# Kernel tuning notes

Hardware: AMD Instinct MI355X
Metric: run time of the kernel (lower is better)

Reference implementation:

```python
import jax, jax.numpy as jnp
import numpy as np

N = 100000   # nodes
H = 96       # hidden_dim
A = 32       # attn_dim
De = 16      # edge_embeddings_dim
E = 500000   # edges per edge type
NEG_SLOPE = 0.01  # torch F.leaky_relu default


def setup_inputs() -> dict:
    key = jax.random.key(0)
    ks = jax.random.split(key, 24)
    nrm = lambda k, shape, s=1.0: jax.random.normal(k, shape, dtype=jnp.float32) * s
    idx = lambda k: jax.random.randint(k, (E,), 0, N, dtype=jnp.int32)
    Din = 2 * H + De
    return {
        'h': nrm(ks[0], (N, H)),
        'src0': idx(ks[1]), 'dst0': idx(ks[2]),
        'src1': idx(ks[3]), 'dst1': idx(ks[4]),
        'src2': idx(ks[5]), 'dst2': idx(ks[6]),
        'Wm0': nrm(ks[7], (Din, H), Din ** -0.5), 'bm0': jnp.zeros((H,), jnp.float32), 'ef0': nrm(ks[8], (De,)),
        'Wm1': nrm(ks[9], (Din, H), Din ** -0.5), 'bm1': jnp.zeros((H,), jnp.float32), 'ef1': nrm(ks[10], (De,)),
        'Wm2': nrm(ks[11], (Din, H), Din ** -0.5), 'bm2': jnp.zeros((H,), jnp.float32), 'ef2': nrm(ks[12], (De,)),
        'Wn0': nrm(ks[13], (H, A), H ** -0.5), 'Wa0': nrm(ks[14], (2 * A, 1), (2 * A) ** -0.5),
        'Wn1': nrm(ks[15], (H, A), H ** -0.5), 'Wa1': nrm(ks[16], (2 * A, 1), (2 * A) ** -0.5),
        'Wu': nrm(ks[17], (4 * H, H), (4 * H) ** -0.5), 'bu': jnp.zeros((H,), jnp.float32),
    }


def _leaky(x):
    return jnp.where(x > 0, x, NEG_SLOPE * x)


def _edge_msg(h, src, dst, Wm, bm, ef):
    # cat(src_h, dst_h, edge_feature) -> Linear  (dropout p=0, eval mode)
    x = jnp.concatenate([h[src], h[dst], jnp.broadcast_to(ef, (src.shape[0], ef.shape[0]))], axis=-1)
    return x @ Wm + bm  # [E, H]


def _mean_agg(m, dst):
    # fn.mean('m','msg'): per-destination mean over incoming edges
    s = jax.ops.segment_sum(m, dst, num_segments=N)
    c = jax.ops.segment_sum(jnp.ones((m.shape[0],), m.dtype), dst, num_segments=N)
    return s / jnp.maximum(c, 1.0)[:, None]


def _attn_agg(scores, m, dst):
    # per-destination softmax over mailbox (variable-size), then weighted sum
    smax = jax.ops.segment_max(scores, dst, num_segments=N)
    ex = jnp.exp(scores - smax[dst])
    den = jax.ops.segment_sum(ex, dst, num_segments=N)
    num = jax.ops.segment_sum(ex[:, None] * m, dst, num_segments=N)
    return num / jnp.maximum(den, 1e-9)[:, None]


def reference(h, src0, dst0, src1, dst1, src2, dst2,
              Wm0, bm0, ef0, Wm1, bm1, ef1, Wm2, bm2, ef2,
              Wn0, Wa0, Wn1, Wa1, Wu, bu):
    # edge type 0: intra_diff (attention), type 1: inter_diff (attention), type 2: intra_lt (mean)
    m0 = _edge_msg(h, src0, dst0, Wm0, bm0, ef0)
    m1 = _edge_msg(h, src1, dst1, Wm1, bm1, ef1)
    m2 = _edge_msg(h, src2, dst2, Wm2, bm2, ef2)

    z0 = h @ Wn0  # [N, A]
    s0 = _leaky(jnp.concatenate([z0[src0], z0[dst0]], axis=-1) @ Wa0)[:, 0]  # [E]
    z1 = h @ Wn1
    s1 = _leaky(jnp.concatenate([z1[src1], z1[dst1]], axis=-1) @ Wa1)[:, 0]

    msg0 = _attn_agg(s0, m0, dst0)   # [N, H]
    msg1 = _attn_agg(s1, m1, dst1)
    msg2 = _mean_agg(m2, dst2)

    # cross_reducer='stack' then concat over edge-type dim -> [N, 3H]
    mcat = jnp.concatenate([msg0, msg1, msg2], axis=-1)
    # cell node update: Linear(cat(h, m)) + ReLU
    return jax.nn.relu(jnp.concatenate([h, mcat], axis=-1) @ Wu + bu)
```

## Files before the change

kernel.cpp:

```cpp
#include <hip/hip_runtime.h>
#include <hip/hip_bf16.h>
#include <cstdint>

#define NN 100000
#define HH 96
#define AD 32
#define DE 16
#define EE 500000
#define NEG 0.01f

#define GSH 10
#define GSZ 1024
#define KB 98
#define CH 4096
#define BPT 123

typedef __bf16 bf16x8 __attribute__((ext_vector_type(8)));
typedef float  f32x4  __attribute__((ext_vector_type(4)));

__device__ __forceinline__ unsigned short f2b(float x) {
    union { float f; unsigned int u; } v; v.f = x;
    unsigned int r = v.u + 0x7fffu + ((v.u >> 16) & 1u);
    return (unsigned short)(r >> 16);
}
__device__ __forceinline__ float b2f(unsigned short h) {
    union { unsigned int u; float f; } v; v.u = ((unsigned int)h) << 16;
    return v.f;
}

__global__ void prep_kernel(const float* Wm0, const float* bm0, const float* ef0,
                            const float* Wm1, const float* bm1, const float* ef1,
                            const float* Wm2, const float* bm2, const float* ef2,
                            const float* Wn0, const float* Wa0,
                            const float* Wn1, const float* Wa1,
                            const float* Wu,
                            float* cvec, float* wvec,
                            unsigned short* BfN, unsigned short* BfU) {
    const float* Wm[3] = {Wm0, Wm1, Wm2};
    const float* bm[3] = {bm0, bm1, bm2};
    const float* ef[3] = {ef0, ef1, ef2};
    const int total = 288 + 384 + 55296 + 36864;
    for (int i = blockIdx.x * blockDim.x + threadIdx.x; i < total;
         i += gridDim.x * blockDim.x) {
        if (i < 288) {
            int t = i / 96, j = i % 96;
            float s = bm[t][j];
            for (int k = 0; k < DE; ++k) s += ef[t][k] * Wm[t][(2 * HH + k) * HH + j];
            cvec[i] = s;
        } else if (i < 288 + 384) {
            int ii = i - 288;
            int kind = ii / 96, k = ii % 96;
            const float* Wn = (kind < 2) ? Wn0 : Wn1;
            const float* Wa = (kind < 2) ? Wa0 : Wa1;
            int off = (kind & 1) ? AD : 0;
            float s = 0.f;
            for (int a = 0; a < AD; ++a) s += Wn[k * AD + a] * Wa[off + a];
            wvec[ii] = s;
        } else if (i < 288 + 384 + 55296) {
            int ii = i - 672;
            int sec = ii / 9216; int rem = ii % 9216;
            int ksc = rem / 512; int lj = rem % 512;
            int ks = ksc / 6, c = ksc % 6;
            int lane = lj / 8, jj = lj % 8;
            int quad = lane / 16, m = lane % 16;
            int k = ks * 32 + quad * 8 + jj;
            int n = c * 16 + m;
            int mt = (sec < 3) ? sec : sec - 3;
            int rowoff = (sec < 3) ? 0 : HH;
            BfN[ii] = f2b(Wm[mt][(rowoff + k) * HH + n]);
        } else {
            int ii = i - (672 + 55296);
            int ksc = ii / 512; int lj = ii % 512;
            int ks = ksc / 6, c = ksc % 6;
            int lane = lj / 8, jj = lj % 8;
            int quad = lane / 16, m = lane % 16;
            int k = ks * 32 + quad * 8 + jj;
            int n = c * 16 + m;
            BfU[ii] = f2b(Wu[k * HH + n]);
        }
    }
}

__global__ void cast_uv_kernel(const float* __restrict__ h, const float* __restrict__ wvec,
                               unsigned short* __restrict__ hb, float* __restrict__ uv) {
    int lane = threadIdx.x & 31;
    int node = (blockIdx.x * blockDim.x + threadIdx.x) >> 5;
    if (node >= NN) return;
    float h0 = h[node * HH + lane];
    float h1 = h[node * HH + 32 + lane];
    float h2 = h[node * HH + 64 + lane];
    hb[node * HH + lane] = f2b(h0);
    hb[node * HH + 32 + lane] = f2b(h1);
    hb[node * HH + 64 + lane] = f2b(h2);
    float acc[4];
#pragma unroll
    for (int q = 0; q < 4; ++q)
        acc[q] = h0 * wvec[q * 96 + lane] + h1 * wvec[q * 96 + 32 + lane] +
                 h2 * wvec[q * 96 + 64 + lane];
#pragma unroll
    for (int d = 16; d >= 1; d >>= 1)
#pragma unroll
        for (int q = 0; q < 4; ++q) acc[q] += __shfl_down(acc[q], d, 32);
    if (lane == 0) {
#pragma unroll
        for (int q = 0; q < 4; ++q) uv[q * NN + node] = acc[q];
    }
}

__global__ void zero_kernel(float4* __restrict__ p, int n4) {
    for (int i = blockIdx.x * blockDim.x + threadIdx.x; i < n4;
         i += gridDim.x * blockDim.x)
        p[i] = make_float4(0.f, 0.f, 0.f, 0.f);
}

__global__ void bucket_hist(const int* __restrict__ d0, const int* __restrict__ d1,
                            const int* __restrict__ d2, int* __restrict__ bCnt) {
    __shared__ int hist[3 * KB];
    int t = threadIdx.x;
    for (int j = t; j < 3 * KB; j += 256) hist[j] = 0;
    __syncthreads();
    const int total = 3 * EE;
    for (int i = blockIdx.x * blockDim.x + t; i < total; i += gridDim.x * blockDim.x) {
        int ty = i / EE, e = i - ty * EE;
        const int* d = (ty == 0) ? d0 : (ty == 1) ? d1 : d2;
        atomicAdd(&hist[ty * KB + (d[e] >> GSH)], 1);
    }
    __syncthreads();
    for (int j = t; j < 3 * KB; j += 256)
        if (hist[j]) atomicAdd(&bCnt[j], hist[j]);
}

__global__ void bucket_scan(const int* __restrict__ bCnt, int* __restrict__ bBase,
                            int* __restrict__ gCursor, int* __restrict__ rs) {
    __shared__ int hist[3 * KB];
    int t = threadIdx.x;
    if (t < 3 * KB) hist[t] = bCnt[t];
    __syncthreads();
    if (t < 3) {
        int run = 0;
        for (int b = 0; b < KB; ++b) {
            bBase[t * (KB + 1) + b] = run;
            gCursor[t * KB + b] = run;
            run += hist[t * KB + b];
        }
        bBase[t * (KB + 1) + KB] = run;
        rs[(size_t)t * (NN + 1) + NN] = run;
    }
}

__global__ __launch_bounds__(256) void bucket_scatter(
    const int* __restrict__ s0, const int* __restrict__ d0,
    const int* __restrict__ s1, const int* __restrict__ d1,
    const int* __restrict__ s2, const int* __restrict__ d2,
    int* __restrict__ gCursor, unsigned int* __restrict__ binned) {
    __shared__ unsigned int recs[CH];
    __shared__ unsigned short rnk[CH];
    __shared__ unsigned char bkt[CH];
    __shared__ int cnt[KB];
    __shared__ int gpos[KB];
    int t = threadIdx.x;
    int type = blockIdx.x / BPT;
    int chunk = (blockIdx.x % BPT) * CH;
    const int* src = (type == 0) ? s0 : (type == 1) ? s1 : s2;
    const int* dst = (type == 0) ? d0 : (type == 1) ? d1 : d2;
    if (t < KB) cnt[t] = 0;
    __syncthreads();
#pragma unroll
    for (int k = 0; k < CH / 256; ++k) {
        int idx = k * 256 + t;
        int e = chunk + idx;
        if (e < EE) {
            int s = src[e], d = dst[e];
            int b = d >> GSH;
            recs[idx] = ((unsigned int)s << GSH) | (unsigned int)(d & (GSZ - 1));
            bkt[idx] = (unsigned char)b;
            rnk[idx] = (unsigned short)atomicAdd(&cnt[b], 1);
        } else {
            bkt[idx] = 0xFF;
        }
    }
    __syncthreads();
    if (t < KB) {
        int c = cnt[t];
        gpos[t] = (c > 0) ? atomicAdd(&gCursor[type * KB + t], c) : 0;
    }
    __syncthreads();
    unsigned int* bout = binned + (size_t)type * EE;
#pragma unroll
    for (int k = 0; k < CH / 256; ++k) {
        int idx = k * 256 + t;
        unsigned char b = bkt[idx];
        if (b != 0xFF) bout[gpos[b] + rnk[idx]] = recs[idx];
    }
}

__global__ __launch_bounds__(256) void bucket_sort(
    const unsigned int* __restrict__ binned, const int* __restrict__ bBase,
    const float* __restrict__ uv,
    int* __restrict__ rs, int* __restrict__ sorted, float* __restrict__ expw) {
    __shared__ int cnt[GSZ];
    __shared__ int tsum[256];
    int t = threadIdx.x;
    int type = blockIdx.x / KB;
    int b = blockIdx.x % KB;
    int nodeBase = b * GSZ;
    int eb = bBase[type * (KB + 1) + b];
    int en = bBase[type * (KB + 1) + b + 1];
    int n = en - eb;
    const unsigned int* bin = binned + (size_t)type * EE + eb;
#pragma unroll
    for (int k = 0; k < GSZ / 256; ++k) cnt[k * 256 + t] = 0;
    __syncthreads();
    for (int i = t; i < n; i += 256) atomicAdd(&cnt[bin[i] & (GSZ - 1)], 1);
    __syncthreads();
    int v[4], s = 0;
#pragma unroll
    for (int k = 0; k < 4; ++k) { v[k] = cnt[t * 4 + k]; s += v[k]; }
    tsum[t] = s;
    __syncthreads();
    for (int off = 1; off < 256; off <<= 1) {
        int add = (t >= off) ? tsum[t - off] : 0;
        __syncthreads();
        tsum[t] += add;
        __syncthreads();
    }
    int run = tsum[t] - s;
    int offk[4];
#pragma unroll
    for (int k = 0; k < 4; ++k) { offk[k] = run; run += v[k]; }
    int* rsrow = rs + (size_t)type * (NN + 1) + nodeBase;
#pragma unroll
    for (int k = 0; k < 4; ++k) {
        int node = t * 4 + k;
        if (nodeBase + node < NN) rsrow[node] = eb + offk[k];
    }
    __syncthreads();
#pragma unroll
    for (int k = 0; k < 4; ++k) cnt[t * 4 + k] = offk[k];
    __syncthreads();
    int* so = sorted + (size_t)type * EE + eb;
    float* ew = expw + (size_t)type * EE + eb;
    const float* u = uv + 2 * type * NN;
    const float* vv = uv + (2 * type + 1) * NN;
    for (int i = t; i < n; i += 256) {
        unsigned int r = bin[i];
        int dl = r & (GSZ - 1);
        int p = atomicAdd(&cnt[dl], 1);
        int srcn = (int)(r >> GSH);
        so[p] = srcn;
        float wgt = 1.f;
        if (type < 2) {
            float sc = u[srcn] + vv[nodeBase + dl];
            sc = sc > 0.f ? sc : NEG * sc;
            wgt = __expf(sc);
        }
        ew[p] = wgt;
    }
}

__global__ void aggregate_kernel(const int* __restrict__ rsAll, const int* __restrict__ sortedAll,
                                 const float* __restrict__ expwAll,
                                 const unsigned short* __restrict__ hb,
                                 unsigned short* __restrict__ hagg,
                                 float* __restrict__ den) {
    const size_t NH = (size_t)NN * HH;
    int lane = threadIdx.x & 31;
    int node = (blockIdx.x * blockDim.x + threadIdx.x) >> 5;
    if (node >= NN) return;
    int t = blockIdx.y;
    const int* rs = rsAll + (size_t)t * (NN + 1);
    const int* sorted = sortedAll + (size_t)t * EE;
    const float* expw = expwAll + (size_t)t * EE;

    int beg = rs[node], end = rs[node + 1];
    float a0 = 0.f, a1 = 0.f, a2 = 0.f, dn = 0.f;
    for (int base = beg; base < end; base += 32) {
        int batch = end - base;
        if (batch > 32) batch = 32;
        int li = lane < batch ? lane : batch - 1;
        int myS = sorted[base + li];
        float myW = expw[base + li];
#pragma unroll 1
        for (int j = 0; j < batch; j += 8) {
            int rem = batch - j;
            int sI[8];
            float wv[8];
#pragma unroll
            for (int k = 0; k < 8; ++k) {
                int jj = (k < rem ? j + k : j);
                sI[k] = __shfl(myS, jj, 32);
                wv[k] = __shfl(myW, jj, 32);
            }
#pragma unroll
            for (int k = 0; k < 8; ++k) if (k >= rem) wv[k] = 0.f;
            float x0[8], x1[8], x2[8];
#pragma unroll
            for (int k = 0; k < 8; ++k) {
                const unsigned short* pr = hb + (size_t)sI[k] * HH;
                x0[k] = b2f(pr[lane]);
                x1[k] = b2f(pr[lane + 32]);
                x2[k] = b2f(pr[lane + 64]);
            }
#pragma unroll
            for (int k = 0; k < 8; ++k) {
                dn += wv[k];
                a0 += wv[k] * x0[k];
                a1 += wv[k] * x1[k];
                a2 += wv[k] * x2[k];
            }
        }
    }
    float r0 = 0.f, r1 = 0.f, r2 = 0.f;
    if (dn > 0.f) {
        float inv = 1.f / dn;
        r0 = a0 * inv; r1 = a1 * inv; r2 = a2 * inv;
    }
    unsigned short* mr = hagg + (size_t)t * NH + (size_t)node * HH;
    mr[lane] = f2b(r0);
    mr[lane + 32] = f2b(r1);
    mr[lane + 64] = f2b(r2);
    if (lane == 0) den[(size_t)t * NN + node] = dn;
}

#define MSP 296
__global__ __launch_bounds__(256) void fused_update_kernel(
    const unsigned short* __restrict__ hagg, const unsigned short* __restrict__ hb,
    const unsigned short* __restrict__ BfN, const unsigned short* __restrict__ BfU,
    const float* __restrict__ den, const float* __restrict__ cvec,
    const float* __restrict__ bu, float* __restrict__ out) {
    __shared__ unsigned short msgt[4][16][MSP];
    const size_t NH = (size_t)NN * HH;
    int wave = threadIdx.x >> 6;
    int lane = threadIdx.x & 63;
    int quad = lane >> 4, m = lane & 15;
    int blk = blockIdx.x * 4 + wave;
    bool active = (blk < NN / 16);
    int r0 = blk * 16;
    bf16x8 hfrag[3];
    if (active) {
        const unsigned short* hrow = hb + (size_t)(r0 + m) * HH + quad * 8;
#pragma unroll
        for (int ks = 0; ks < 3; ++ks) hfrag[ks] = *(const bf16x8*)(hrow + ks * 32);
#pragma unroll
        for (int t = 0; t < 3; ++t) {
            f32x4 acc[6] = {};
            const unsigned short* harow = hagg + (size_t)t * NH + (size_t)(r0 + m) * HH + quad * 8;
#pragma unroll
            for (int ks = 0; ks < 3; ++ks) {
                bf16x8 af = *(const bf16x8*)(harow + ks * 32);
#pragma unroll
                for (int c = 0; c < 6; ++c) {
                    bf16x8 bfv = *(const bf16x8*)(BfN + (((t * 3 + ks) * 6 + c) << 9) + lane * 8);
                    acc[c] = __builtin_amdgcn_mfma_f32_16x16x32_bf16(af, bfv, acc[c], 0, 0, 0);
                }
            }
#pragma unroll
            for (int ks = 0; ks < 3; ++ks) {
#pragma unroll
                for (int c = 0; c < 6; ++c) {
                    bf16x8 bfv = *(const bf16x8*)(BfN + ((((t + 3) * 3 + ks) * 6 + c) << 9) + lane * 8);
                    acc[c] = __builtin_amdgcn_mfma_f32_16x16x32_bf16(hfrag[ks], bfv, acc[c], 0, 0, 0);
                }
            }
            float dnv[4];
#pragma unroll
            for (int r = 0; r < 4; ++r) dnv[r] = den[(size_t)t * NN + r0 + quad * 4 + r];
#pragma unroll
            for (int c = 0; c < 6; ++c) {
                float cv = cvec[t * 96 + c * 16 + m];
#pragma unroll
                for (int r = 0; r < 4; ++r) {
                    float val = (dnv[r] > 0.f) ? (acc[c][r] + cv) : 0.f;
                    msgt[wave][quad * 4 + r][t * 96 + c * 16 + m] = f2b(val);
                }
            }
        }
    }
    __syncthreads();
    if (active) {
        f32x4 acc2[6] = {};
#pragma unroll
        for (int ks = 0; ks < 12; ++ks) {
            bf16x8 af = (ks < 3) ? hfrag[ks]
                                 : *(const bf16x8*)&msgt[wave][m][(ks - 3) * 32 + quad * 8];
#pragma unroll
            for (int c = 0; c < 6; ++c) {
                bf16x8 bfv = *(const bf16x8*)(BfU + ((ks * 6 + c) << 9) + lane * 8);
                acc2[c] = __builtin_amdgcn_mfma_f32_16x16x32_bf16(af, bfv, acc2[c], 0, 0, 0);
            }
        }
#pragma unroll
        for (int c = 0; c < 6; ++c) {
            float b = bu[c * 16 + m];
#pragma unroll
            for (int r = 0; r < 4; ++r) {
                int row = r0 + quad * 4 + r;
                float v2 = acc2[c][r] + b;
                out[(size_t)row * HH + c * 16 + m] = v2 > 0.f ? v2 : 0.f;
            }
        }
    }
}

extern "C" void kernel_launch(void* const* d_in, const int* in_sizes, int n_in,
                              void* d_out, int out_size, void* d_ws, size_t ws_size,
                              hipStream_t stream) {
    (void)in_sizes; (void)n_in; (void)out_size;
    const float* h   = (const float*)d_in[0];
    const int* srcs[3] = {(const int*)d_in[1], (const int*)d_in[3], (const int*)d_in[5]};
    const int* dsts[3] = {(const int*)d_in[2], (const int*)d_in[4], (const int*)d_in[6]};
    const float* Wm0 = (const float*)d_in[7];
    const float* bm0 = (const float*)d_in[8];
    const float* ef0 = (const float*)d_in[9];
    const float* Wm1 = (const float*)d_in[10];
    const float* bm1 = (const float*)d_in[11];
    const float* ef1 = (const float*)d_in[12];
    const float* Wm2 = (const float*)d_in[13];
    const float* bm2 = (const float*)d_in[14];
    const float* ef2 = (const float*)d_in[15];
    const float* Wn0 = (const float*)d_in[16];
    const float* Wa0 = (const float*)d_in[17];
    const float* Wn1 = (const float*)d_in[18];
    const float* Wa1 = (const float*)d_in[19];
    const float* Wu  = (const float*)d_in[20];
    const float* bu  = (const float*)d_in[21];
    float* out = (float*)d_out;

    const size_t NEED = 98991104;
    if (ws_size < NEED) return;
    char* w = (char*)d_ws;
    unsigned short* hb      = (unsigned short*)(w + 0);
    unsigned short* hagg    = (unsigned short*)(w + 19200000);
    float*          den     = (float*)(w + 76800000);
    float*          uv      = (float*)(w + 78000000);
    float*          cvec    = (float*)(w + 79600000);
    float*          wvec    = (float*)(w + 79601280);
    unsigned short* BfN     = (unsigned short*)(w + 79602816);
    unsigned short* BfU     = (unsigned short*)(w + 79713408);
    int*            bBase   = (int*)(w + 79787136);
    int*            gCursor = (int*)(w + 79788416);
    int*            bCnt    = (int*)(w + 79789696);
    int*            rs      = (int*)(w + 79790976);
    int*            sorted  = (int*)(w + 80991104);
    unsigned int*   binned  = (unsigned int*)(w + 86991104);
    float*          expw    = (float*)(w + 92991104);

    prep_kernel<<<128, 256, 0, stream>>>(Wm0, bm0, ef0, Wm1, bm1, ef1, Wm2, bm2, ef2,
                                         Wn0, Wa0, Wn1, Wa1, Wu, cvec, wvec, BfN, BfU);
    cast_uv_kernel<<<12500, 256, 0, stream>>>(h, wvec, hb, uv);

    zero_kernel<<<1, 256, 0, stream>>>((float4*)bCnt, 80);
    bucket_hist<<<512, 256, 0, stream>>>(dsts[0], dsts[1], dsts[2], bCnt);
    bucket_scan<<<1, 384, 0, stream>>>(bCnt, bBase, gCursor, rs);
    bucket_scatter<<<3 * BPT, 256, 0, stream>>>(srcs[0], dsts[0], srcs[1], dsts[1],
                                                srcs[2], dsts[2], gCursor, binned);
    bucket_sort<<<3 * KB, 256, 0, stream>>>(binned, bBase, uv, rs, sorted, expw);

    aggregate_kernel<<<dim3(12500, 3), 256, 0, stream>>>(rs, sorted, expw, hb, hagg, den);
    fused_update_kernel<<<1563, 256, 0, stream>>>(hagg, hb, BfN, BfU, den, cvec, bu, out);
}
```

Measured before the change: 346.7 us.

## Fold message weights into update weights and merge front-end kernels

Precomputes the products Wm_t·Wu_t, so the output kernel does one fused set of MFMAs per edge type and no longer needs the intermediate message tile in shared memory or a second GEMM pass. Merges the bf16 cast, attention-vector computation, weight prep and destination histogram into a single kernel launch. The histogram now writes per-block partials that the scan sums, which removes the zero kernel and the global atomics. In exchange, the prep blocks do heavier dot products serially, and rounding the folded weights to bf16 changes numerics slightly.

New measurement: 397.8 us. 14.7% more time.

```diff
diff --git a/kernel.cpp b/kernel.cpp
--- a/kernel.cpp
+++ b/kernel.cpp
@@ -15,6 +15,10 @@
 #define CH 4096
 #define BPT 123
 
+#define FB_CAST 12500
+#define FB_PREP 128
+#define FB_HIST 64
+
 typedef __bf16 bf16x8 __attribute__((ext_vector_type(8)));
 typedef float  f32x4  __attribute__((ext_vector_type(4)));
 
@@ -28,113 +32,121 @@
     return v.f;
 }
 
-__global__ void prep_kernel(const float* Wm0, const float* bm0, const float* ef0,
-                            const float* Wm1, const float* bm1, const float* ef1,
-                            const float* Wm2, const float* bm2, const float* ef2,
-                            const float* Wn0, const float* Wa0,
-                            const float* Wn1, const float* Wa1,
-                            const float* Wu,
-                            float* cvec, float* wvec,
-                            unsigned short* BfN, unsigned short* BfU) {
-    const float* Wm[3] = {Wm0, Wm1, Wm2};
-    const float* bm[3] = {bm0, bm1, bm2};
-    const float* ef[3] = {ef0, ef1, ef2};
-    const int total = 288 + 384 + 55296 + 36864;
-    for (int i = blockIdx.x * blockDim.x + threadIdx.x; i < total;
-         i += gridDim.x * blockDim.x) {
-        if (i < 288) {
-            int t = i / 96, j = i % 96;
-            float s = bm[t][j];
-            for (int k = 0; k < DE; ++k) s += ef[t][k] * Wm[t][(2 * HH + k) * HH + j];
-            cvec[i] = s;
-        } else if (i < 288 + 384) {
-            int ii = i - 288;
+__global__ __launch_bounds__(256) void fused_front(
+    const float* __restrict__ h,
+    const float* __restrict__ Wm0, const float* __restrict__ bm0, const float* __restrict__ ef0,
+    const float* __restrict__ Wm1, const float* __restrict__ bm1, const float* __restrict__ ef1,
+    const float* __restrict__ Wm2, const float* __restrict__ bm2, const float* __restrict__ ef2,
+    const float* __restrict__ Wn0, const float* __restrict__ Wa0,
+    const float* __restrict__ Wn1, const float* __restrict__ Wa1,
+    const float* __restrict__ Wu,
+    const int* __restrict__ d0, const int* __restrict__ d1, const int* __restrict__ d2,
+    unsigned short* __restrict__ hb, float* __restrict__ uv,
+    unsigned short* __restrict__ BfC, float* __restrict__ cu,
+    int* __restrict__ bCntPart) {
+    int bid = blockIdx.x;
+    int tid = threadIdx.x;
+    if (bid < FB_CAST) {
+        __shared__ float wl[384];
+        for (int ii = tid; ii < 384; ii += 256) {
             int kind = ii / 96, k = ii % 96;
             const float* Wn = (kind < 2) ? Wn0 : Wn1;
             const float* Wa = (kind < 2) ? Wa0 : Wa1;
             int off = (kind & 1) ? AD : 0;
             float s = 0.f;
             for (int a = 0; a < AD; ++a) s += Wn[k * AD + a] * Wa[off + a];
-            wvec[ii] = s;
-        } else if (i < 288 + 384 + 55296) {
-            int ii = i - 672;
-            int sec = ii / 9216; int rem = ii % 9216;
-            int ksc = rem / 512; int lj = rem % 512;
-            int ks = ksc / 6, c = ksc % 6;
-            int lane = lj / 8, jj = lj % 8;
-            int quad = lane / 16, m = lane % 16;
-            int k = ks * 32 + quad * 8 + jj;
-            int n = c * 16 + m;
-            int mt = (sec < 3) ? sec : sec - 3;
-            int rowoff = (sec < 3) ? 0 : HH;
-            BfN[ii] = f2b(Wm[mt][(rowoff + k) * HH + n]);
-        } else {
-            int ii = i - (672 + 55296);
-            int ksc = ii / 512; int lj = ii % 512;
-            int ks = ksc / 6, c = ksc % 6;
-            int lane = lj / 8, jj = lj % 8;
-            int quad = lane / 16, m = lane % 16;
-            int k = ks * 32 + quad * 8 + jj;
-            int n = c * 16 + m;
-            BfU[ii] = f2b(Wu[k * HH + n]);
-        }
-    }
-}
-
-__global__ void cast_uv_kernel(const float* __restrict__ h, const float* __restrict__ wvec,
-                               unsigned short* __restrict__ hb, float* __restrict__ uv) {
-    int lane = threadIdx.x & 31;
-    int node = (blockIdx.x * blockDim.x + threadIdx.x) >> 5;
-    if (node >= NN) return;
-    float h0 = h[node * HH + lane];
-    float h1 = h[node * HH + 32 + lane];
-    float h2 = h[node * HH + 64 + lane];
-    hb[node * HH + lane] = f2b(h0);
-    hb[node * HH + 32 + lane] = f2b(h1);
-    hb[node * HH + 64 + lane] = f2b(h2);
-    float acc[4];
-#pragma unroll
-    for (int q = 0; q < 4; ++q)
-        acc[q] = h0 * wvec[q * 96 + lane] + h1 * wvec[q * 96 + 32 + lane] +
-                 h2 * wvec[q * 96 + 64 + lane];
-#pragma unroll
-    for (int d = 16; d >= 1; d >>= 1)
-#pragma unroll
-        for (int q = 0; q < 4; ++q) acc[q] += __shfl_down(acc[q], d, 32);
-    if (lane == 0) {
-#pragma unroll
-        for (int q = 0; q < 4; ++q) uv[q * NN + node] = acc[q];
-    }
-}
-
-__global__ void zero_kernel(float4* __restrict__ p, int n4) {
-    for (int i = blockIdx.x * blockDim.x + threadIdx.x; i < n4;
-         i += gridDim.x * blockDim.x)
-        p[i] = make_float4(0.f, 0.f, 0.f, 0.f);
-}
-
-__global__ void bucket_hist(const int* __restrict__ d0, const int* __restrict__ d1,
-                            const int* __restrict__ d2, int* __restrict__ bCnt) {
-    __shared__ int hist[3 * KB];
-    int t = threadIdx.x;
-    for (int j = t; j < 3 * KB; j += 256) hist[j] = 0;
-    __syncthreads();
-    const int total = 3 * EE;
-    for (int i = blockIdx.x * blockDim.x + t; i < total; i += gridDim.x * blockDim.x) {
-        int ty = i / EE, e = i - ty * EE;
-        const int* d = (ty == 0) ? d0 : (ty == 1) ? d1 : d2;
-        atomicAdd(&hist[ty * KB + (d[e] >> GSH)], 1);
-    }
-    __syncthreads();
-    for (int j = t; j < 3 * KB; j += 256)
-        if (hist[j]) atomicAdd(&bCnt[j], hist[j]);
-}
-
-__global__ void bucket_scan(const int* __restrict__ bCnt, int* __restrict__ bBase,
+            wl[ii] = s;
+        }
+        __syncthreads();
+        int lane = tid & 31;
+        int node = (bid * 256 + tid) >> 5;
+        float h0 = h[node * HH + lane];
+        float h1 = h[node * HH + 32 + lane];
+        float h2 = h[node * HH + 64 + lane];
+        hb[node * HH + lane] = f2b(h0);
+        hb[node * HH + 32 + lane] = f2b(h1);
+        hb[node * HH + 64 + lane] = f2b(h2);
+        float acc[4];
+#pragma unroll
+        for (int q = 0; q < 4; ++q)
+            acc[q] = h0 * wl[q * 96 + lane] + h1 * wl[q * 96 + 32 + lane] +
+                     h2 * wl[q * 96 + 64 + lane];
+#pragma unroll
+        for (int d = 16; d >= 1; d >>= 1)
+#pragma unroll
+            for (int q = 0; q < 4; ++q) acc[q] += __shfl_down(acc[q], d, 32);
+        if (lane == 0) {
+#pragma unroll
+            for (int q = 0; q < 4; ++q) uv[q * NN + node] = acc[q];
+        }
+    } else if (bid < FB_CAST + FB_PREP) {
+        const float* Wm[3] = {Wm0, Wm1, Wm2};
+        const float* bm[3] = {bm0, bm1, bm2};
+        const float* ef[3] = {ef0, ef1, ef2};
+        const int total = 7 * 9216 + 288;
+        for (int i = (bid - FB_CAST) * 256 + tid; i < total; i += FB_PREP * 256) {
+            if (i < 7 * 9216) {
+                int sec = i / 9216, rem = i % 9216;
+                int ksc = rem / 512, lj = rem % 512;
+                int ks = ksc / 6, c = ksc % 6;
+                int lane = lj / 8, j = lj % 8;
+                int quad = lane / 16, mm = lane % 16;
+                int k = ks * 32 + quad * 8 + j;
+                int n = c * 16 + mm;
+                float val;
+                if (sec == 0) {
+                    val = Wu[k * HH + n];
+                } else if (sec < 4) {
+                    int t = sec - 1;
+                    const float* W = Wm[t];
+                    val = 0.f;
+                    for (int jj = 0; jj < 96; ++jj)
+                        val += W[k * HH + jj] * Wu[(96 + 96 * t + jj) * HH + n];
+                } else {
+                    int t = sec - 4;
+                    const float* W = Wm[t];
+                    val = 0.f;
+                    for (int jj = 0; jj < 96; ++jj)
+                        val += W[(96 + k) * HH + jj] * Wu[(96 + 96 * t + jj) * HH + n];
+                }
+                BfC[i] = f2b(val);
+            } else {
+                int ii = i - 7 * 9216;
+                int t = ii / 96, n = ii % 96;
+                float s = 0.f;
+                for (int k = 0; k < 96; ++k) {
+                    float ct = bm[t][k];
+                    for (int j = 0; j < DE; ++j) ct += ef[t][j] * Wm[t][(192 + j) * HH + k];
+                    s += ct * Wu[(96 + 96 * t + k) * HH + n];
+                }
+                cu[ii] = s;
+            }
+        }
+    } else {
+        __shared__ int hl[3 * KB];
+        int hblk = bid - (FB_CAST + FB_PREP);
+        for (int j = tid; j < 3 * KB; j += 256) hl[j] = 0;
+        __syncthreads();
+        const int total = 3 * EE;
+        for (int i = hblk * 256 + tid; i < total; i += FB_HIST * 256) {
+            int ty = i / EE, e = i - ty * EE;
+            const int* d = (ty == 0) ? d0 : (ty == 1) ? d1 : d2;
+            atomicAdd(&hl[ty * KB + (d[e] >> GSH)], 1);
+        }
+        __syncthreads();
+        for (int j = tid; j < 3 * KB; j += 256) bCntPart[hblk * (3 * KB) + j] = hl[j];
+    }
+}
+
+__global__ void bucket_scan(const int* __restrict__ bCntPart, int* __restrict__ bBase,
                             int* __restrict__ gCursor, int* __restrict__ rs) {
     __shared__ int hist[3 * KB];
     int t = threadIdx.x;
-    if (t < 3 * KB) hist[t] = bCnt[t];
+    if (t < 3 * KB) {
+        int s = 0;
+        for (int b = 0; b < FB_HIST; ++b) s += bCntPart[b * (3 * KB) + t];
+        hist[t] = s;
+    }
     __syncthreads();
     if (t < 3) {
         int run = 0;
@@ -322,82 +334,69 @@
     if (lane == 0) den[(size_t)t * NN + node] = dn;
 }
 
-#define MSP 296
-__global__ __launch_bounds__(256) void fused_update_kernel(
+__global__ __launch_bounds__(256) void fused_out_kernel(
     const unsigned short* __restrict__ hagg, const unsigned short* __restrict__ hb,
-    const unsigned short* __restrict__ BfN, const unsigned short* __restrict__ BfU,
-    const float* __restrict__ den, const float* __restrict__ cvec,
-    const float* __restrict__ bu, float* __restrict__ out) {
-    __shared__ unsigned short msgt[4][16][MSP];
+    const unsigned short* __restrict__ BfC, const float* __restrict__ cu,
+    const float* __restrict__ den, const float* __restrict__ bu,
+    float* __restrict__ out) {
     const size_t NH = (size_t)NN * HH;
     int wave = threadIdx.x >> 6;
     int lane = threadIdx.x & 63;
     int quad = lane >> 4, m = lane & 15;
     int blk = blockIdx.x * 4 + wave;
-    bool active = (blk < NN / 16);
+    if (blk >= NN / 16) return;
     int r0 = blk * 16;
     bf16x8 hfrag[3];
-    if (active) {
-        const unsigned short* hrow = hb + (size_t)(r0 + m) * HH + quad * 8;
-#pragma unroll
-        for (int ks = 0; ks < 3; ++ks) hfrag[ks] = *(const bf16x8*)(hrow + ks * 32);
-#pragma unroll
-        for (int t = 0; t < 3; ++t) {
-            f32x4 acc[6] = {};
-            const unsigned short* harow = hagg + (size_t)t * NH + (size_t)(r0 + m) * HH + quad * 8;
-#pragma unroll
-            for (int ks = 0; ks < 3; ++ks) {
-                bf16x8 af = *(const bf16x8*)(harow + ks * 32);
-#pragma unroll
-                for (int c = 0; c < 6; ++c) {
-                    bf16x8 bfv = *(const bf16x8*)(BfN + (((t * 3 + ks) * 6 + c) << 9) + lane * 8);
-                    acc[c] = __builtin_amdgcn_mfma_f32_16x16x32_bf16(af, bfv, acc[c], 0, 0, 0);
-                }
-            }
-#pragma unroll
-            for (int ks = 0; ks < 3; ++ks) {
-#pragma unroll
-                for (int c = 0; c < 6; ++c) {
-                    bf16x8 bfv = *(const bf16x8*)(BfN + ((((t + 3) * 3 + ks) * 6 + c) << 9) + lane * 8);
-                    acc[c] = __builtin_amdgcn_mfma_f32_16x16x32_bf16(hfrag[ks], bfv, acc[c], 0, 0, 0);
-                }
-            }
-            float dnv[4];
-#pragma unroll
-            for (int r = 0; r < 4; ++r) dnv[r] = den[(size_t)t * NN + r0 + quad * 4 + r];
+    const unsigned short* hrow = hb + (size_t)(r0 + m) * HH + quad * 8;
+#pragma unroll
+    for (int ks = 0; ks < 3; ++ks) hfrag[ks] = *(const bf16x8*)(hrow + ks * 32);
+    f32x4 tot[6] = {};
+#pragma unroll
+    for (int ks = 0; ks < 3; ++ks)
+#pragma unroll
+        for (int c = 0; c < 6; ++c) {
+            bf16x8 bfv = *(const bf16x8*)(BfC + ((ks * 6 + c) << 9) + lane * 8);
+            tot[c] = __builtin_amdgcn_mfma_f32_16x16x32_bf16(hfrag[ks], bfv, tot[c], 0, 0, 0);
+        }
+#pragma unroll
+    for (int t = 0; t < 3; ++t) {
+        f32x4 ta[6] = {};
+        const unsigned short* harow = hagg + (size_t)t * NH + (size_t)(r0 + m) * HH + quad * 8;
+#pragma unroll
+        for (int ks = 0; ks < 3; ++ks) {
+            bf16x8 af = *(const bf16x8*)(harow + ks * 32);
 #pragma unroll
             for (int c = 0; c < 6; ++c) {
-                float cv = cvec[t * 96 + c * 16 + m];
-#pragma unroll
-                for (int r = 0; r < 4; ++r) {
-                    float val = (dnv[r] > 0.f) ? (acc[c][r] + cv) : 0.f;
-                    msgt[wave][quad * 4 + r][t * 96 + c * 16 + m] = f2b(val);
-                }
-            }
-        }
-    }
-    __syncthreads();
-    if (active) {
-        f32x4 acc2[6] = {};
-#pragma unroll
-        for (int ks = 0; ks < 12; ++ks) {
-            bf16x8 af = (ks < 3) ? hfrag[ks]
-                                 : *(const bf16x8*)&msgt[wave][m][(ks - 3) * 32 + quad * 8];
+                bf16x8 bfv = *(const bf16x8*)(BfC + (1 + t) * 9216 + ((ks * 6 + c) << 9) + lane * 8);
+                ta[c] = __builtin_amdgcn_mfma_f32_16x16x32_bf16(af, bfv, ta[c], 0, 0, 0);
+            }
+        }
+#pragma unroll
+        for (int ks = 0; ks < 3; ++ks)
 #pragma unroll
             for (int c = 0; c < 6; ++c) {
-                bf16x8 bfv = *(const bf16x8*)(BfU + ((ks * 6 + c) << 9) + lane * 8);
-                acc2[c] = __builtin_amdgcn_mfma_f32_16x16x32_bf16(af, bfv, acc2[c], 0, 0, 0);
-            }
-        }
+                bf16x8 bfv = *(const bf16x8*)(BfC + (4 + t) * 9216 + ((ks * 6 + c) << 9) + lane * 8);
+                ta[c] = __builtin_amdgcn_mfma_f32_16x16x32_bf16(hfrag[ks], bfv, ta[c], 0, 0, 0);
+            }
+        float dnv[4];
+#pragma unroll
+        for (int r = 0; r < 4; ++r) dnv[r] = den[(size_t)t * NN + r0 + quad * 4 + r];
 #pragma unroll
         for (int c = 0; c < 6; ++c) {
-            float b = bu[c * 16 + m];
-#pragma unroll
-            for (int r = 0; r < 4; ++r) {
-                int row = r0 + quad * 4 + r;
-                float v2 = acc2[c][r] + b;
-                out[(size_t)row * HH + c * 16 + m] = v2 > 0.f ? v2 : 0.f;
-            }
+            float cv = cu[t * 96 + c * 16 + m];
+#pragma unroll
+            for (int r = 0; r < 4; ++r)
+                if (dnv[r] > 0.f) tot[c][r] += ta[c][r] + cv;
+        }
+    }
+#pragma unroll
+    for (int c = 0; c < 6; ++c) {
+        float b = bu[c * 16 + m];
+#pragma unroll
+        for (int r = 0; r < 4; ++r) {
+            int row = r0 + quad * 4 + r;
+            float v2 = tot[c][r] + b;
+            out[(size_t)row * HH + c * 16 + m] = v2 > 0.f ? v2 : 0.f;
         }
     }
 }
@@ -426,36 +425,31 @@
     const float* bu  = (const float*)d_in[21];
     float* out = (float*)d_out;
 
-    const size_t NEED = 98991104;
+    const size_t NEED = 99011200;
     if (ws_size < NEED) return;
     char* w = (char*)d_ws;
-    unsigned short* hb      = (unsigned short*)(w + 0);
-    unsigned short* hagg    = (unsigned short*)(w + 19200000);
-    float*          den     = (float*)(w + 76800000);
-    float*          uv      = (float*)(w + 78000000);
-    float*          cvec    = (float*)(w + 79600000);
-    float*          wvec    = (float*)(w + 79601280);
-    unsigned short* BfN     = (unsigned short*)(w + 79602816);
-    unsigned short* BfU     = (unsigned short*)(w + 79713408);
-    int*            bBase   = (int*)(w + 79787136);
-    int*            gCursor = (int*)(w + 79788416);
-    int*            bCnt    = (int*)(w + 79789696);
-    int*            rs      = (int*)(w + 79790976);
-    int*            sorted  = (int*)(w + 80991104);
-    unsigned int*   binned  = (unsigned int*)(w + 86991104);
-    float*          expw    = (float*)(w + 92991104);
-
-    prep_kernel<<<128, 256, 0, stream>>>(Wm0, bm0, ef0, Wm1, bm1, ef1, Wm2, bm2, ef2,
-                                         Wn0, Wa0, Wn1, Wa1, Wu, cvec, wvec, BfN, BfU);
-    cast_uv_kernel<<<12500, 256, 0, stream>>>(h, wvec, hb, uv);
-
-    zero_kernel<<<1, 256, 0, stream>>>((float4*)bCnt, 80);
-    bucket_hist<<<512, 256, 0, stream>>>(dsts[0], dsts[1], dsts[2], bCnt);
-    bucket_scan<<<1, 384, 0, stream>>>(bCnt, bBase, gCursor, rs);
+    unsigned short* hb       = (unsigned short*)(w + 0);
+    unsigned short* hagg     = (unsigned short*)(w + 19200000);
+    float*          den      = (float*)(w + 76800000);
+    float*          uv       = (float*)(w + 78000000);
+    float*          cu       = (float*)(w + 79600000);
+    unsigned short* BfC      = (unsigned short*)(w + 79601152);
+    int*            bBase    = (int*)(w + 79731200);
+    int*            gCursor  = (int*)(w + 79732480);
+    int*            bCntPart = (int*)(w + 79733760);
+    int*            rs       = (int*)(w + 79810560);
+    int*            sorted   = (int*)(w + 81011200);
+    unsigned int*   binned   = (unsigned int*)(w + 87011200);
+    float*          expw     = (float*)(w + 93011200);
+
+    fused_front<<<FB_CAST + FB_PREP + FB_HIST, 256, 0, stream>>>(
+        h, Wm0, bm0, ef0, Wm1, bm1, ef1, Wm2, bm2, ef2,
+        Wn0, Wa0, Wn1, Wa1, Wu, dsts[0], dsts[1], dsts[2],
+        hb, uv, BfC, cu, bCntPart);
+    bucket_scan<<<1, 384, 0, stream>>>(bCntPart, bBase, gCursor, rs);
     bucket_scatter<<<3 * BPT, 256, 0, stream>>>(srcs[0], dsts[0], srcs[1], dsts[1],
                                                 srcs[2], dsts[2], gCursor, binned);
     bucket_sort<<<3 * KB, 256, 0, stream>>>(binned, bBase, uv, rs, sorted, expw);
-
     aggregate_kernel<<<dim3(12500, 3), 256, 0, stream>>>(rs, sorted, expw, hb, hagg, den);
-    fused_update_kernel<<<1563, 256, 0, stream>>>(hagg, hb, BfN, BfU, den, cvec, bu, out);
-}
+    fused_out_kernel<<<1563, 256, 0, stream>>>(hagg, hb, BfC, cu, den, bu, out);
+}
```
